# Performance work log

Hardware: AMD Instinct MI355X
Metric: run time of the kernel (lower is better)

## Reference

```python
import jax, jax.numpy as jnp
import numpy as np

D_MODEL = 1024
N_HEADS = 16
D_KV = 64
INNER = N_HEADS * D_KV  # 1024


def setup_inputs() -> dict:
    key = jax.random.key(0)
    ks = jax.random.split(key, 6)
    B, SV, ST = 4, 1024, 1024
    vis = jax.random.normal(ks[0], (B, SV, D_MODEL), dtype=jnp.float32)
    txt = jax.random.normal(ks[1], (B, ST, D_MODEL), dtype=jnp.float32)
    s = 0.02
    Wq = jax.random.normal(ks[2], (D_MODEL, INNER), dtype=jnp.float32) * s
    Wk = jax.random.normal(ks[3], (D_MODEL, INNER), dtype=jnp.float32) * s
    Wv = jax.random.normal(ks[4], (D_MODEL, INNER), dtype=jnp.float32) * s
    Wo = jax.random.normal(ks[5], (INNER, D_MODEL), dtype=jnp.float32) * s
    return {"vis_hidden_states": vis, "txt_hidden_states": txt,
            "Wq": Wq, "Wk": Wk, "Wv": Wv, "Wo": Wo}


def _split_heads(x):
    # [B, S, INNER] -> [B, H, S, Dk]
    B, S, _ = x.shape
    return x.reshape(B, S, N_HEADS, D_KV).transpose(0, 2, 1, 3)


def _merge_heads(x):
    # [B, H, S, Dk] -> [B, S, INNER]
    B, H, S, Dk = x.shape
    return x.transpose(0, 2, 1, 3).reshape(B, S, H * Dk)


def reference(vis_hidden_states, txt_hidden_states, Wq, Wk, Wv, Wo):
    # T5-style attention: NO 1/sqrt(d) scaling, no biases.
    q = _split_heads(vis_hidden_states @ Wq)   # [B,H,Sv,Dk]
    k = _split_heads(txt_hidden_states @ Wk)   # [B,H,St,Dk]
    v = _split_heads(txt_hidden_states @ Wv)   # [B,H,St,Dk]
    v2 = _split_heads(vis_hidden_states @ Wv)  # [B,H,Sv,Dk]

    scores = jnp.einsum('bhqd,bhkd->bhqk', q, k)  # [B,H,Sv,St]
    attn = jax.nn.softmax(scores.astype(jnp.float32), axis=-1).astype(scores.dtype)

    vis_out = jnp.einsum('bhqk,bhkd->bhqd', attn, v)   # softmax-normalized over k
    txt_out = jnp.einsum('bhqk,bhqd->bhkd', attn, v2)  # transposed attn, NOT renormalized

    vis_out = _merge_heads(vis_out) @ Wo  # [B,Sv,D]
    txt_out = _merge_heads(txt_out) @ Wo  # [B,St,D]
    return vis_out, txt_out
```

## Files before the change

### kernel.cpp

```cpp
#include <hip/hip_runtime.h>

typedef unsigned short u16;
typedef unsigned int u32;
typedef __bf16 bf16x8 __attribute__((ext_vector_type(8)));
typedef float f32x4 __attribute__((ext_vector_type(4)));
typedef u16 u16x4 __attribute__((ext_vector_type(4)));
typedef __attribute__((address_space(1))) void* as1_t;
typedef __attribute__((address_space(3))) void* as3_t;

#define LOG2E 1.4426950408889634f
#define MFMA(a,b,c) __builtin_amdgcn_mfma_f32_16x16x32_bf16(a,b,c,0,0,0)

__device__ __forceinline__ u16 f2bf(float f){
  u32 u = __float_as_uint(f);
  return (u16)((u + 0x7FFFu + ((u >> 16) & 1u)) >> 16);
}
__device__ __forceinline__ float bf2f(u16 x){
  return __uint_as_float(((u32)x) << 16);
}
#if __has_builtin(__builtin_amdgcn_cvt_pk_bf16_f32)
__device__ __forceinline__ u16x4 pk4(float a, float b, float c, float d){
  auto lo = __builtin_amdgcn_cvt_pk_bf16_f32(a,b);
  auto hi = __builtin_amdgcn_cvt_pk_bf16_f32(c,d);
  union { u16x4 v; u32 w[2]; } u;
  u.w[0] = __builtin_bit_cast(u32, lo);
  u.w[1] = __builtin_bit_cast(u32, hi);
  return u.v;
}
#else
__device__ __forceinline__ u16x4 pk4(float a, float b, float c, float d){
  u16x4 r = { f2bf(a), f2bf(b), f2bf(c), f2bf(d) };
  return r;
}
#endif
__device__ __forceinline__ void gld16(const u16* gp, u16* lp){
  __builtin_amdgcn_global_load_lds((as1_t)(u16*)gp, (as3_t)lp, 16, 0, 0);
}

#define SBAR  __builtin_amdgcn_s_barrier()
#define SCHB  __builtin_amdgcn_sched_barrier(0)
#define SP1   __builtin_amdgcn_s_setprio(1)
#define SP0   __builtin_amdgcn_s_setprio(0)
#define WAITL0 asm volatile("s_waitcnt lgkmcnt(0)" ::: "memory")
#define WAITV6 asm volatile("s_waitcnt vmcnt(6)" ::: "memory")
#define WV8 asm volatile("s_waitcnt vmcnt(8)" ::: "memory")

__global__ void prep_kernel(const float* __restrict__ vis, u16* __restrict__ vis16,
                            const float* __restrict__ txt, u16* __restrict__ txt16,
                            const float* __restrict__ Wq, const float* __restrict__ Wk,
                            const float* __restrict__ Wv, const float* __restrict__ Wo,
                            u16* __restrict__ T0, u16* __restrict__ T1,
                            u16* __restrict__ T2, u16* __restrict__ T3,
                            u16* __restrict__ T4){
  int bid = blockIdx.x;
  if(bid < 8192){
    const float* src = (bid < 4096) ? vis : txt;
    u16* dst = (bid < 4096) ? vis16 : txt16;
    int idx = ((bid & 4095)*256 + threadIdx.x)*4;
    float4 v = *(const float4*)(src + idx);
    *(u16x4*)(dst + idx) = pk4(v.x, v.y, v.z, v.w);
    return;
  }
  int rr = bid - 8192;
  int wi = rr >> 8, tile = rr & 255;
  const float* W; u16* WT;
  switch(wi){
    case 0: W = Wq; WT = T0; break;
    case 1: W = Wv; WT = T1; break;
    case 2: W = Wk; WT = T2; break;
    case 3: W = Wv; WT = T3; break;
    default: W = Wo; WT = T4; break;
  }
  __shared__ u16 t[64][65];
  int bn = (tile & 15)*64, bk = (tile >> 4)*64;
  int c = threadIdx.x & 63, r0 = threadIdx.x >> 6;
  #pragma unroll
  for(int j=0;j<64;j+=4){
    int r = r0 + j;
    t[r][c] = f2bf(W[(bk + r)*1024 + bn + c]);
  }
  __syncthreads();
  #pragma unroll
  for(int j=0;j<64;j+=4){
    int r = r0 + j;
    WT[(bn + r)*1024 + bk + c] = t[c][r];
  }
}

#define STG(G, gbase, dsto, kk) { \
    _Pragma("unroll") \
    for(int ii=0;ii<4;ii++){ \
      int slot_ = ii*512 + tid; int r_ = slot_ >> 3, cs_ = slot_ & 7; \
      gld16((G) + (size_t)((gbase) + r_)*1024 + (kk) + ((cs_ ^ (r_ & 7)) << 3), \
            lds + (dsto) + (ii*512 + (w << 6))*8); } }

#define LDA_(bo, mh) { \
    _Pragma("unroll") \
    for(int q_=0;q_<4;q_++){ \
      int ro_ = (bo) + arow + (((mh)*4 + q_) << 10); \
      af[q_][0] = *(const bf16x8*)(lds + ro_ + sx0); \
      af[q_][1] = *(const bf16x8*)(lds + ro_ + sx1); } }

#define LDB_(bo, nh, bfv) { \
    _Pragma("unroll") \
    for(int j_=0;j_<2;j_++){ \
      int ro_ = (bo) + brow + (((nh)*2 + j_) << 10); \
      bfv[j_][0] = *(const bf16x8*)(lds + ro_ + sx0); \
      bfv[j_][1] = *(const bf16x8*)(lds + ro_ + sx1); } }

#define MM_N(mh, bfv, nh) { \
    _Pragma("unroll") \
    for(int q_=0;q_<4;q_++) \
      _Pragma("unroll") \
      for(int j_=0;j_<2;j_++){ \
        int ai_ = ((mh)*4+q_)*4 + (nh)*2+j_; \
        acc[ai_] = MFMA(af[q_][0], bfv[j_][0], acc[ai_]); \
        acc[ai_] = MFMA(af[q_][1], bfv[j_][1], acc[ai_]); } }

#define MM_T(mh, bfv, nh) { \
    _Pragma("unroll") \
    for(int q_=0;q_<4;q_++) \
      _Pragma("unroll") \
      for(int j_=0;j_<2;j_++){ \
        int ai_ = ((nh)*2+j_)*8 + (mh)*4+q_; \
        acc[ai_] = MFMA(bfv[j_][0], af[q_][0], acc[ai_]); \
        acc[ai_] = MFMA(bfv[j_][1], af[q_][1], acc[ai_]); } }

#define TILE_BODY(bufo, ts, MM) { \
    LDA_(bufo, 0); LDB_(bufo, 0, bfv0); \
    SBAR; WAITL0; SCHB; SP1; MM(0, bfv0, 0); SP0; SBAR; \
    LDB_(bufo, 1, bfv1); \
    SBAR; WAITL0; SCHB; SP1; MM(0, bfv1, 1); SP0; SBAR; \
    LDA_(bufo, 1); \
    SBAR; WAITL0; SCHB; SP1; MM(1, bfv1, 1); SP0; SBAR; \
    STG(A , bm, (bufo)        , ts); \
    STG(Bt, bn, (bufo) + 16384, ts); \
    SCHB; SP1; MM(1, bfv0, 0); SP0; \
    WV8; SBAR; }

__global__ __launch_bounds__(512, 2)
void proj_gemm_kernel(const u16* __restrict__ Avis, const u16* __restrict__ Atxt,
                      const u16* __restrict__ Wvis, const u16* __restrict__ Wtxt,
                      u16* __restrict__ Qb, u16* __restrict__ V2t,
                      u16* __restrict__ Kb, u16* __restrict__ Vt)
{
  const u16 *A, *Bt; u16 *Cn, *Ct;
  if(blockIdx.z == 0){ A = Avis; Bt = Wvis; Cn = Qb; Ct = V2t; }
  else               { A = Atxt; Bt = Wtxt; Cn = Kb; Ct = Vt;  }
  __shared__ u16 lds[65536];
  const int tid = threadIdx.x, w = tid >> 6, lane = tid & 63;
  const int quad = lane >> 4, cl = lane & 15;
  const int wr = w >> 2, wc = w & 3;
  const int bm = blockIdx.x*256, bn = blockIdx.y*256;
  const int sx0 = ((quad    ) ^ (cl & 7)) << 3;
  const int sx1 = ((quad + 4) ^ (cl & 7)) << 3;
  const int arow = ((wr << 7) + cl) << 6;
  const int brow = (((wc << 6) + cl) << 6) + 16384;

  f32x4 acc[32];
  #pragma unroll
  for(int a=0;a<32;a++){ f32x4 z = {0.f,0.f,0.f,0.f}; acc[a] = z; }
  bf16x8 af[4][2], bfv0[2][2], bfv1[2][2];

  STG(A , bm, 0,     0);  STG(Bt, bn, 16384, 0);
  STG(A , bm, 32768, 64); STG(Bt, bn, 32768+16384, 64);
  WV8; SBAR;

  if(bn < 1024){
    for(int tt=0; tt<8; tt++){
      const int t0 = 2*tt;
      TILE_BODY(0,     ((t0+2)&15) << 6, MM_N);
      TILE_BODY(32768, ((t0+3)&15) << 6, MM_N);
    }
    #pragma unroll
    for(int mf=0; mf<8; mf++){
      int m0 = bm + wr*128 + mf*16 + quad*4;
      #pragma unroll
      for(int nf=0; nf<4; nf++){
        int n = bn + wc*64 + nf*16 + cl;
        int h = n >> 6, d = n & 63;
        #pragma unroll
        for(int i2=0;i2<4;i2++){
          int m = m0 + i2; int b = m >> 10, s = m & 1023;
          Cn[(((size_t)(b*16 + h)*1024 + s) << 6) + d] = f2bf(acc[mf*4+nf][i2]);
        }
      }
    }
  } else {
    for(int tt=0; tt<8; tt++){
      const int t0 = 2*tt;
      TILE_BODY(0,     ((t0+2)&15) << 6, MM_T);
      TILE_BODY(32768, ((t0+3)&15) << 6, MM_T);
    }
    const int bT = bm >> 10;
    const int sbase = (bm & 1023) + wr*128;
    #pragma unroll
    for(int nf=0; nf<4; nf++){
      #pragma unroll
      for(int i2=0;i2<4;i2++){
        int nn = (bn - 1024) + wc*64 + nf*16 + quad*4 + i2;
        int h = nn >> 6, d = nn & 63;
        u16* rowp = Ct + ((size_t)(bT*16 + h)*64 + d)*1024;
        #pragma unroll
        for(int mf=0; mf<8; mf++)
          rowp[sbase + mf*16 + cl] = f2bf(acc[nf*8+mf][i2]);
      }
    }
  }
}

#undef STG
#undef LDA_
#undef LDB_
#undef MM_N
#undef MM_T
#undef TILE_BODY

__device__ __forceinline__ void gemm_pipe(const u16* __restrict__ A,
                                          const u16* __restrict__ Bt,
                                          int bm, int bn,
                                          u16* __restrict__ lds,
                                          f32x4 (&acc)[4][4],
                                          int tid, int w, int quad, int cl,
                                          int wr, int wc)
{
  const int sx0 = ((quad    ) ^ (cl & 7)) << 3;
  const int sx1 = ((quad + 4) ^ (cl & 7)) << 3;
  const int arow = ((wr << 6) + cl) << 6;
  const int brow = (((wc << 6) + cl) << 6) + 16384;
  bf16x8 af[4][2], bfv[2][2];

#define STAGE128(G, gbase, dsto, kk) { \
    _Pragma("unroll") \
    for(int ii=0;ii<2;ii++){ \
      int slot_ = ii*512 + tid; int r_ = slot_ >> 3, cs_ = slot_ & 7; \
      gld16((G) + (size_t)((gbase) + r_)*1024 + (kk) + ((cs_ ^ (r_ & 7)) << 3), \
            lds + (dsto) + (ii*512 + (w << 6))*8); } }

#define LDA_(bo) { \
    _Pragma("unroll") \
    for(int m_=0;m_<4;m_++){ \
      int ro_ = (bo) + arow + (m_ << 10); \
      af[m_][0] = *(const bf16x8*)(lds + ro_ + sx0); \
      af[m_][1] = *(const bf16x8*)(lds + ro_ + sx1); } }

#define LDB_(bo, nh) { \
    _Pragma("unroll") \
    for(int j_=0;j_<2;j_++){ \
      int ro_ = (bo) + brow + (((nh)*2 + j_) << 10); \
      bfv[j_][0] = *(const bf16x8*)(lds + ro_ + sx0); \
      bfv[j_][1] = *(const bf16x8*)(lds + ro_ + sx1); } }

#define MM_(nh) { \
    _Pragma("unroll") \
    for(int m_=0;m_<4;m_++) \
      _Pragma("unroll") \
      for(int j_=0;j_<2;j_++){ \
        acc[m_][(nh)*2+j_] = MFMA(af[m_][0], bfv[j_][0], acc[m_][(nh)*2+j_]); \
        acc[m_][(nh)*2+j_] = MFMA(af[m_][1], bfv[j_][1], acc[m_][(nh)*2+j_]); } }

  STAGE128(A , bm      , 0,          0);
  STAGE128(A , bm + 128, 8192,       0);
  STAGE128(Bt, bn      , 16384,      0);
  STAGE128(A , bm      , 24576,      64);
  STAGE128(A , bm + 128, 24576+8192, 64);
  STAGE128(Bt, bn      , 24576+16384,64);
  WAITV6; SBAR;

  #pragma unroll 2
  for(int t=0;t<16;t++){
    const int c  = (t % 3) * 24576;
    const int n2 = ((t+2) % 3) * 24576;
    const int ts = ((t+2) & 15) << 6;
    LDA_(c); LDB_(c, 0);
    STAGE128(A, bm      , n2,        ts);
    STAGE128(A, bm + 128, n2 + 8192, ts);
    SBAR; WAITL0; SCHB;
    SP1; MM_(0); SP0;
    SBAR;
    LDB_(c, 1);
    STAGE128(Bt, bn, n2 + 16384, ts);
    SBAR; WAITL0; SCHB;
    SP1; MM_(1); SP0;
    WAITV6;
    SBAR;
  }
#undef STAGE128
#undef LDA_
#undef LDB_
#undef MM_
}

__global__ __launch_bounds__(512, 2)
void out_gemm_kernel(const u16* __restrict__ A, const u16* __restrict__ Bt,
                     float* __restrict__ Cf)
{
  __shared__ u16 lds[73728];
  const int tid = threadIdx.x, w = tid >> 6, lane = tid & 63;
  const int quad = lane >> 4, cl = lane & 15;
  const int wr = w >> 1, wc = w & 1;
  const int bm = blockIdx.x*256, bn = blockIdx.y*128;

  f32x4 acc[4][4];
  #pragma unroll
  for(int a=0;a<4;a++)
    #pragma unroll
    for(int b=0;b<4;b++){ f32x4 z = {0.f,0.f,0.f,0.f}; acc[a][b] = z; }

  gemm_pipe(A, Bt, bm, bn, lds, acc, tid, w, quad, cl, wr, wc);

  #pragma unroll
  for(int mf=0; mf<4; mf++)
    #pragma unroll
    for(int nf=0; nf<4; nf++)
      #pragma unroll
      for(int i=0;i<4;i++){
        int m = bm + wr*64 + mf*16 + quad*4 + i;
        int n = bn + wc*64 + nf*16 + cl;
        Cf[(size_t)m*1024 + n] = acc[mf][nf][i];
      }
}

__global__ __launch_bounds__(512, 4)
void attn_vis_kernel(const u16* __restrict__ Q, const u16* __restrict__ Kc,
                     const u16* __restrict__ Vt, u16* __restrict__ visA,
                     float* __restrict__ rl_g)
{
  __shared__ u16 lds[17408];
  u16* Pl  = lds;
  u16* Kst = lds + 9216;
  u16* Vst = lds + 13312;
  const int tid = threadIdx.x, w = tid>>6, lane = tid&63;
  const int quad = lane>>4, cl = lane&15;
  const int bh = blockIdx.x, q0 = blockIdx.y*128;
  const u16* Qh  = Q  + (size_t)bh*65536;
  const u16* Kh  = Kc + (size_t)bh*65536;
  const u16* Vth = Vt + (size_t)bh*65536;

  #pragma unroll
  for(int i=0;i<2;i++){
    int slot = i*512 + tid;
    int c = slot >> 7, r = slot & 127;
    gld16(Qh + (size_t)(q0 + r)*64 + c*8, Pl + slot*8);
  }
  __syncthreads();
  bf16x8 qf[2];
  #pragma unroll
  for(int kk=0;kk<2;kk++)
    qf[kk] = *(const bf16x8*)(Pl + ((kk*4+quad)*128 + w*16 + cl)*8);
  __syncthreads();

  float lrun = 0.f;
  f32x4 oacc[4];
  #pragma unroll
  for(int dt=0;dt<4;dt++){ f32x4 z = {0.f,0.f,0.f,0.f}; oacc[dt] = z; }

  for(int kt=0;kt<16;kt++){
    __syncthreads();
    {
      int slot = tid;
      { int c = slot >> 6, r = slot & 63;
        gld16(Kh + (size_t)(kt*64 + r)*64 + c*8, Kst + slot*8); }
      { int d = slot >> 3, ch = slot & 7;
        gld16(Vth + (size_t)d*1024 + kt*64 + (ch^(d&7))*8, Vst + slot*8); }
    }
    __syncthreads();
    #pragma unroll
    for(int mtk=0;mtk<4;mtk++){
      f32x4 s = {0.f,0.f,0.f,0.f};
      #pragma unroll
      for(int kk=0;kk<2;kk++){
        bf16x8 ka = *(const bf16x8*)(Kst + ((kk*4+quad)*64 + mtk*16 + cl)*8);
        s = MFMA(ka, qf[kk], s);
      }
      float p0 = __builtin_amdgcn_exp2f(s[0]*LOG2E);
      float p1 = __builtin_amdgcn_exp2f(s[1]*LOG2E);
      float p2 = __builtin_amdgcn_exp2f(s[2]*LOG2E);
      float p3 = __builtin_amdgcn_exp2f(s[3]*LOG2E);
      lrun += (p0+p1)+(p2+p3);
      *(u16x4*)(Pl + (w*16 + cl)*72 + mtk*16 + quad*4) = pk4(p0,p1,p2,p3);
    }
    bf16x8 pa[2];
    #pragma unroll
    for(int kk=0;kk<2;kk++)
      pa[kk] = *(const bf16x8*)(Pl + (w*16 + cl)*72 + kk*32 + quad*8);
    #pragma unroll
    for(int dt=0;dt<4;dt++){
      int d = dt*16 + cl;
      #pragma unroll
      for(int kk=0;kk<2;kk++){
        bf16x8 vb = *(const bf16x8*)(Vst + d*64 + (((kk*4+quad)^(d&7))*8));
        oacc[dt] = MFMA(pa[kk], vb, oacc[dt]);
      }
    }
  }
  lrun += __shfl_xor(lrun, 16, 64);
  lrun += __shfl_xor(lrun, 32, 64);
  float rl = 1.f/lrun;
  if(quad == 0) rl_g[bh*1024 + q0 + w*16 + cl] = rl;
  const int b = bh >> 4, h = bh & 15;
  #pragma unroll
  for(int i=0;i<4;i++){
    float rr = __shfl(rl, quad*4 + i, 16);
    int q = q0 + w*16 + quad*4 + i;
    #pragma unroll
    for(int dt=0;dt<4;dt++)
      visA[(size_t)(b*1024 + q)*1024 + h*64 + dt*16 + cl] = f2bf(oacc[dt][i]*rr);
  }
}

__global__ __launch_bounds__(512, 4)
void attn_txt_kernel(const u16* __restrict__ Kc, const u16* __restrict__ Q,
                     const u16* __restrict__ V2t, const float* __restrict__ rl_g,
                     u16* __restrict__ txtA)
{
  __shared__ u16 lds[17408];
  u16* Pl  = lds;
  u16* Qst = lds + 9216;
  u16* Vst = lds + 13312;
  const int tid = threadIdx.x, w = tid>>6, lane = tid&63;
  const int quad = lane>>4, cl = lane&15;
  const int bh = blockIdx.x, k0 = blockIdx.y*128;
  const u16* Kh  = Kc  + (size_t)bh*65536;
  const u16* Qh  = Q   + (size_t)bh*65536;
  const u16* Vth = V2t + (size_t)bh*65536;

  #pragma unroll
  for(int i=0;i<2;i++){
    int slot = i*512 + tid;
    int c = slot >> 7, r = slot & 127;
    gld16(Kh + (size_t)(k0 + r)*64 + c*8, Pl + slot*8);
  }
  __syncthreads();
  bf16x8 kb[2];
  #pragma unroll
  for(int kk=0;kk<2;kk++)
    kb[kk] = *(const bf16x8*)(Pl + ((kk*4+quad)*128 + w*16 + cl)*8);
  __syncthreads();

  f32x4 oacc[4];
  #pragma unroll
  for(int dt=0;dt<4;dt++){ f32x4 z = {0.f,0.f,0.f,0.f}; oacc[dt] = z; }

  for(int qt=0;qt<16;qt++){
    __syncthreads();
    {
      int slot = tid;
      { int c = slot >> 6, r = slot & 63;
        gld16(Qh + (size_t)(qt*64 + r)*64 + c*8, Qst + slot*8); }
      { int d = slot >> 3, ch = slot & 7;
        gld16(Vth + (size_t)d*1024 + qt*64 + (ch^(d&7))*8, Vst + slot*8); }
    }
    __syncthreads();
    f32x4 rv[4];
    #pragma unroll
    for(int mtq=0;mtq<4;mtq++)
      rv[mtq] = *(const f32x4*)(rl_g + bh*1024 + qt*64 + mtq*16 + quad*4);
    #pragma unroll
    for(int mtq=0;mtq<4;mtq++){
      f32x4 s = {0.f,0.f,0.f,0.f};
      #pragma unroll
      for(int kk=0;kk<2;kk++){
        bf16x8 qa = *(const bf16x8*)(Qst + ((kk*4+quad)*64 + mtq*16 + cl)*8);
        s = MFMA(qa, kb[kk], s);
      }
      float p0 = __builtin_amdgcn_exp2f(s[0]*LOG2E)*rv[mtq][0];
      float p1 = __builtin_amdgcn_exp2f(s[1]*LOG2E)*rv[mtq][1];
      float p2 = __builtin_amdgcn_exp2f(s[2]*LOG2E)*rv[mtq][2];
      float p3 = __builtin_amdgcn_exp2f(s[3]*LOG2E)*rv[mtq][3];
      *(u16x4*)(Pl + (w*16 + cl)*72 + mtq*16 + quad*4) = pk4(p0,p1,p2,p3);
    }
    bf16x8 pa[2];
    #pragma unroll
    for(int kk=0;kk<2;kk++)
      pa[kk] = *(const bf16x8*)(Pl + (w*16 + cl)*72 + kk*32 + quad*8);
    #pragma unroll
    for(int dt=0;dt<4;dt++){
      int d = dt*16 + cl;
      #pragma unroll
      for(int kk=0;kk<2;kk++){
        bf16x8 vb = *(const bf16x8*)(Vst + d*64 + (((kk*4+quad)^(d&7))*8));
        oacc[dt] = MFMA(pa[kk], vb, oacc[dt]);
      }
    }
  }
  const int b = bh >> 4, h = bh & 15;
  #pragma unroll
  for(int i=0;i<4;i++){
    int k = k0 + w*16 + quad*4 + i;
    #pragma unroll
    for(int dt=0;dt<4;dt++)
      txtA[(size_t)(b*1024 + k)*1024 + h*64 + dt*16 + cl] = f2bf(oacc[dt][i]);
  }
}

extern "C" void kernel_launch(void* const* d_in, const int* in_sizes, int n_in,
                              void* d_out, int out_size, void* d_ws, size_t ws_size,
                              hipStream_t stream)
{
  const float* vis = (const float*)d_in[0];
  const float* txt = (const float*)d_in[1];
  const float* Wq  = (const float*)d_in[2];
  const float* Wk  = (const float*)d_in[3];
  const float* Wv  = (const float*)d_in[4];
  const float* Wo  = (const float*)d_in[5];
  float* out = (float*)d_out;

  char* ws = (char*)d_ws;
  const size_t MB = 1u << 20;
  u16* vis16 = (u16*)(ws + 0);
  u16* txt16 = (u16*)(ws + 8*MB);
  u16* Wvis  = (u16*)(ws + 16*MB);
  u16* Wtxt  = (u16*)(ws + 20*MB);
  u16* Qb    = (u16*)(ws + 24*MB);
  u16* Kb    = (u16*)(ws + 32*MB);
  u16* Vt    = (u16*)(ws + 40*MB);
  u16* V2t   = (u16*)(ws + 48*MB);
  float* rl_g = (float*)(ws + 56*MB);
  u16* WoT   = (u16*)(ws + 57*MB);
  u16* visA = vis16;  u16* txtA = txt16;

  prep_kernel<<<9472, 256, 0, stream>>>(vis, vis16, txt, txt16,
                                        Wq, Wk, Wv, Wo,
                                        Wvis, Wvis + 1048576, Wtxt, Wtxt + 1048576, WoT);
  proj_gemm_kernel<<<dim3(16,8,2), 512, 0, stream>>>(vis16, txt16, Wvis, Wtxt,
                                                     Qb, V2t, Kb, Vt);
  attn_vis_kernel<<<dim3(64,8), 512, 0, stream>>>(Qb, Kb, Vt, visA, rl_g);
  attn_txt_kernel<<<dim3(64,8), 512, 0, stream>>>(Kb, Qb, V2t, rl_g, txtA);
  out_gemm_kernel<<<dim3(32,8), 512, 0, stream>>>(visA, WoT, out);
}
```

Measured before the change: 218.3 us.

## Double-buffer K/V and Q/V tiles in attention kernels, stage rl in LDS

Both attention kernels now keep two LDS buffers for the streamed K/V (or Q/V2) tiles and issue the loads for tile t+2 while tile t+1 is already resident. This lets the global-to-LDS transfers overlap with MFMA compute instead of stalling behind a full barrier on every iteration. The txt kernel also copies its per-row reciprocal softmax sums into LDS once, rather than reading them from global memory on every iteration. LDS use per block grows, which may cut the number of resident blocks per CU. The last two iterations redundantly reload an already-used tile.

```diff
diff --git a/kernel.cpp b/kernel.cpp
--- a/kernel.cpp
+++ b/kernel.cpp
@@ -43,6 +43,7 @@
 #define SP0   __builtin_amdgcn_s_setprio(0)
 #define WAITL0 asm volatile("s_waitcnt lgkmcnt(0)" ::: "memory")
 #define WAITV6 asm volatile("s_waitcnt vmcnt(6)" ::: "memory")
+#define WV2 asm volatile("s_waitcnt vmcnt(2)" ::: "memory")
 #define WV8 asm volatile("s_waitcnt vmcnt(8)" ::: "memory")
 
 __global__ void prep_kernel(const float* __restrict__ vis, u16* __restrict__ vis16,
@@ -326,10 +327,8 @@
                      const u16* __restrict__ Vt, u16* __restrict__ visA,
                      float* __restrict__ rl_g)
 {
-  __shared__ u16 lds[17408];
+  __shared__ u16 lds[25600];
   u16* Pl  = lds;
-  u16* Kst = lds + 9216;
-  u16* Vst = lds + 13312;
   const int tid = threadIdx.x, w = tid>>6, lane = tid&63;
   const int quad = lane>>4, cl = lane&15;
   const int bh = blockIdx.x, q0 = blockIdx.y*128;
@@ -350,21 +349,25 @@
     qf[kk] = *(const bf16x8*)(Pl + ((kk*4+quad)*128 + w*16 + cl)*8);
   __syncthreads();
 
+#define KVST(kt, buf) { \
+    u16* B_ = lds + 9216 + (buf)*8192; \
+    { int c_ = tid >> 6, r_ = tid & 63; \
+      gld16(Kh + (size_t)((kt)*64 + r_)*64 + c_*8, B_ + tid*8); } \
+    { int d_ = tid >> 3, ch_ = tid & 7; \
+      gld16(Vth + (size_t)d_*1024 + (kt)*64 + ((ch_^(d_&7))*8), B_ + 4096 + tid*8); } }
+
+  KVST(0, 0); KVST(1, 1);
+  WV2; SBAR;
+
   float lrun = 0.f;
   f32x4 oacc[4];
   #pragma unroll
   for(int dt=0;dt<4;dt++){ f32x4 z = {0.f,0.f,0.f,0.f}; oacc[dt] = z; }
 
   for(int kt=0;kt<16;kt++){
-    __syncthreads();
-    {
-      int slot = tid;
-      { int c = slot >> 6, r = slot & 63;
-        gld16(Kh + (size_t)(kt*64 + r)*64 + c*8, Kst + slot*8); }
-      { int d = slot >> 3, ch = slot & 7;
-        gld16(Vth + (size_t)d*1024 + kt*64 + (ch^(d&7))*8, Vst + slot*8); }
-    }
-    __syncthreads();
+    const int bb = kt & 1;
+    u16* Kst = lds + 9216 + bb*8192;
+    u16* Vst = Kst + 4096;
     #pragma unroll
     for(int mtk=0;mtk<4;mtk++){
       f32x4 s = {0.f,0.f,0.f,0.f};
@@ -393,7 +396,13 @@
         oacc[dt] = MFMA(pa[kk], vb, oacc[dt]);
       }
     }
-  }
+    SBAR;
+    const int nk = (kt < 14) ? kt + 2 : kt;
+    KVST(nk, bb);
+    WV2;
+    SBAR;
+  }
+#undef KVST
   lrun += __shfl_xor(lrun, 16, 64);
   lrun += __shfl_xor(lrun, 32, 64);
   float rl = 1.f/lrun;
@@ -414,10 +423,10 @@
                      const u16* __restrict__ V2t, const float* __restrict__ rl_g,
                      u16* __restrict__ txtA)
 {
-  __shared__ u16 lds[17408];
+  __shared__ u16 lds[27648];
   u16* Pl  = lds;
-  u16* Qst = lds + 9216;
-  u16* Vst = lds + 13312;
+  u16* rlL = lds + 25600;
+  const float* rlF = (const float*)rlL;
   const int tid = threadIdx.x, w = tid>>6, lane = tid&63;
   const int quad = lane>>4, cl = lane&15;
   const int bh = blockIdx.x, k0 = blockIdx.y*128;
@@ -431,6 +440,8 @@
     int c = slot >> 7, r = slot & 127;
     gld16(Kh + (size_t)(k0 + r)*64 + c*8, Pl + slot*8);
   }
+  if(tid < 256)
+    gld16((const u16*)(rl_g + (size_t)bh*1024) + tid*8, rlL + tid*8);
   __syncthreads();
   bf16x8 kb[2];
   #pragma unroll
@@ -438,24 +449,28 @@
     kb[kk] = *(const bf16x8*)(Pl + ((kk*4+quad)*128 + w*16 + cl)*8);
   __syncthreads();
 
+#define QVST(qt, buf) { \
+    u16* B_ = lds + 9216 + (buf)*8192; \
+    { int c_ = tid >> 6, r_ = tid & 63; \
+      gld16(Qh + (size_t)((qt)*64 + r_)*64 + c_*8, B_ + tid*8); } \
+    { int d_ = tid >> 3, ch_ = tid & 7; \
+      gld16(Vth + (size_t)d_*1024 + (qt)*64 + ((ch_^(d_&7))*8), B_ + 4096 + tid*8); } }
+
+  QVST(0, 0); QVST(1, 1);
+  WV2; SBAR;
+
   f32x4 oacc[4];
   #pragma unroll
   for(int dt=0;dt<4;dt++){ f32x4 z = {0.f,0.f,0.f,0.f}; oacc[dt] = z; }
 
   for(int qt=0;qt<16;qt++){
-    __syncthreads();
-    {
-      int slot = tid;
-      { int c = slot >> 6, r = slot & 63;
-        gld16(Qh + (size_t)(qt*64 + r)*64 + c*8, Qst + slot*8); }
-      { int d = slot >> 3, ch = slot & 7;
-        gld16(Vth + (size_t)d*1024 + qt*64 + (ch^(d&7))*8, Vst + slot*8); }
-    }
-    __syncthreads();
+    const int bb = qt & 1;
+    u16* Qst = lds + 9216 + bb*8192;
+    u16* Vst = Qst + 4096;
     f32x4 rv[4];
     #pragma unroll
     for(int mtq=0;mtq<4;mtq++)
-      rv[mtq] = *(const f32x4*)(rl_g + bh*1024 + qt*64 + mtq*16 + quad*4);
+      rv[mtq] = *(const f32x4*)(rlF + qt*64 + mtq*16 + quad*4);
     #pragma unroll
     for(int mtq=0;mtq<4;mtq++){
       f32x4 s = {0.f,0.f,0.f,0.f};
@@ -483,7 +498,13 @@
         oacc[dt] = MFMA(pa[kk], vb, oacc[dt]);
       }
     }
-  }
+    SBAR;
+    const int nq = (qt < 14) ? qt + 2 : qt;
+    QVST(nq, bb);
+    WV2;
+    SBAR;
+  }
+#undef QVST
   const int b = bh >> 4, h = bh & 15;
   #pragma unroll
   for(int i=0;i<4;i++){
```

Result: no change. 214.9 us (-1.6%).
